# Performance work log

Measured on AMD Instinct MI355X. Metric: run time of the kernel, lower is better.

Reference implementation:

```python
import jax, jax.numpy as jnp
import numpy as np

B, D_IN, D_H = 4096, 1024, 1024


def setup_inputs() -> dict:
    key = jax.random.key(0)
    ks = jax.random.split(key, 11)
    s = 1.0 / np.sqrt(D_IN + D_H)  # torch Linear default init scale
    inp = {
        "x": jax.random.normal(ks[0], (B, D_IN), jnp.float32),
        "h": jax.random.normal(ks[1], (B, D_H), jnp.float32),
        "c": jax.random.normal(ks[2], (B, D_H), jnp.float32),
        "W_f": jax.random.uniform(ks[3], (D_IN + D_H, D_H), jnp.float32, -s, s),
        "b_f": jax.random.uniform(ks[4], (D_H,), jnp.float32, -s, s),
        "W_i": jax.random.uniform(ks[5], (D_IN + D_H, D_H), jnp.float32, -s, s),
        "b_i": jax.random.uniform(ks[6], (D_H,), jnp.float32, -s, s),
        "W_c": jax.random.uniform(ks[7], (D_IN + D_H, D_H), jnp.float32, -s, s),
        "b_c": jax.random.uniform(ks[8], (D_H,), jnp.float32, -s, s),
        "W_o": jax.random.uniform(ks[9], (D_IN + D_H, D_H), jnp.float32, -s, s),
        "b_o": jax.random.uniform(ks[10], (D_H,), jnp.float32, -s, s),
    }
    return inp


def reference(x, h, c, W_f, b_f, W_i, b_i, W_c, b_c, W_o, b_o):
    xh = jnp.concatenate([x, h], axis=1)  # [B, D_IN+D_H]
    # fuse four gate linears into one GEMM: [B, 2H] @ [2H, 4H]
    W = jnp.concatenate([W_f, W_i, W_c, W_o], axis=1)
    b = jnp.concatenate([b_f, b_i, b_c, b_o], axis=0)
    gates = xh @ W + b  # [B, 4H]
    f_g, i_g, c_g, o_g = jnp.split(gates, 4, axis=1)
    f = jax.nn.sigmoid(f_g)
    i = jax.nn.sigmoid(i_g)
    ct = jnp.tanh(c_g)
    ot = jax.nn.sigmoid(o_g)
    c_new = f * c + i * ct
    h_new = ot * jnp.tanh(c_new)
    return (h_new, (h_new, c_new))
```

## Files before the change

### kernel.cpp

```cpp
#include <hip/hip_runtime.h>
#include <hip/hip_bf16.h>
#include <cstdint>

typedef __bf16 bf16x8 __attribute__((ext_vector_type(8)));
typedef float f32x4 __attribute__((ext_vector_type(4)));

#define BROWS 4096
#define DH    1024
#define KDIM  2048
#define NT    32

__global__ __launch_bounds__(256) void k_prep(const float* __restrict__ x,
                                              const float* __restrict__ h,
                                              const float* __restrict__ Wf,
                                              const float* __restrict__ Wi,
                                              const float* __restrict__ Wc,
                                              const float* __restrict__ Wo,
                                              __hip_bfloat16* __restrict__ xh,
                                              __hip_bfloat16* __restrict__ wt) {
  __shared__ float t[64][65];
  const int tid = threadIdx.x;
  if (blockIdx.x < 4096) {
    int64_t idx = ((int64_t)blockIdx.x * 256 + tid) * 8;
    int row = (int)(idx >> 11);
    int col = (int)(idx & 2047);
    const float* src = (col < 1024) ? (x + (int64_t)row * 1024 + col)
                                    : (h + (int64_t)row * 1024 + (col - 1024));
    float4 v0 = reinterpret_cast<const float4*>(src)[0];
    float4 v1 = reinterpret_cast<const float4*>(src)[1];
    alignas(16) __hip_bfloat16 o8[8];
    o8[0] = __float2bfloat16(v0.x); o8[1] = __float2bfloat16(v0.y);
    o8[2] = __float2bfloat16(v0.z); o8[3] = __float2bfloat16(v0.w);
    o8[4] = __float2bfloat16(v1.x); o8[5] = __float2bfloat16(v1.y);
    o8[6] = __float2bfloat16(v1.z); o8[7] = __float2bfloat16(v1.w);
    *reinterpret_cast<int4*>(xh + idx) = *reinterpret_cast<const int4*>(o8);
  } else {
    const int b = blockIdx.x - 4096;
    const int g  = b & 3;
    const int jt = (b >> 2) & 15;
    const int kt = b >> 6;
    const float* W = (g == 0) ? Wf : (g == 1) ? Wi : (g == 2) ? Wc : Wo;
    const int j0 = jt << 6, k0 = kt << 6;
#pragma unroll
    for (int i = 0; i < 4; ++i) {
      int r = (tid >> 4) + (i << 4);
      int c = (tid & 15) << 2;
      float4 v = *reinterpret_cast<const float4*>(W + (int64_t)(k0 + r) * 1024 + j0 + c);
      t[r][c + 0] = v.x; t[r][c + 1] = v.y; t[r][c + 2] = v.z; t[r][c + 3] = v.w;
    }
    __syncthreads();
#pragma unroll
    for (int i = 0; i < 2; ++i) {
      int task = tid + (i << 8);
      int rr = task >> 3;
      int kc = (task & 7) << 3;
      int np = (((jt << 2) + (rr >> 4)) << 6) + (g << 4) + (rr & 15);
      alignas(16) __hip_bfloat16 o8[8];
#pragma unroll
      for (int e = 0; e < 8; ++e) o8[e] = __float2bfloat16(t[kc + e][rr]);
      *reinterpret_cast<int4*>(wt + (int64_t)np * KDIM + k0 + kc) =
          *reinterpret_cast<const int4*>(o8);
    }
  }
}

__device__ __forceinline__ float sig_(float v) {
  return __builtin_amdgcn_rcpf(1.0f + __expf(-v));
}
__device__ __forceinline__ float tanh_(float v) {
  return fmaf(2.0f, __builtin_amdgcn_rcpf(1.0f + __expf(-2.0f * v)), -1.0f);
}

#define GLD(PTR, LOFF)                                                           \
  __builtin_amdgcn_global_load_lds(                                              \
      (const __attribute__((address_space(1))) void*)(PTR),                      \
      (__attribute__((address_space(3))) void*)(lds + (LOFF) + wslot), 16, 0, 0)

#define STG2(LP, KH_, PA, PB)                                                    \
  do {                                                                           \
    GLD((PA), (LP) + (KH_) * 8192);                                              \
    GLD((PA) + 128 * KDIM, (LP) + (KH_) * 8192 + 4096);                          \
    GLD((PB), (LP) + 16384 + (KH_) * 8192);                                      \
    GLD((PB) + 128 * KDIM, (LP) + 16384 + (KH_) * 8192 + 4096);                  \
  } while (0)

#define LDSA(P, KH, MI)                                                          \
  (*reinterpret_cast<const bf16x8*>(lds + (P) * 32768 + (KH) * 8192 + abase + (MI) * 512))
#define LDSB(P, KH, NI)                                                          \
  (*reinterpret_cast<const bf16x8*>(lds + (P) * 32768 + (KH) * 8192 + bbase + (NI) * 512))

#define VM4 asm volatile("s_waitcnt vmcnt(4)" ::: "memory")

#define RD_AV(BANK, P_, KH_, H_)                                                 \
  _Pragma("unroll") for (int i = 0; i < 4; ++i) BANK[i] = LDSA(P_, KH_, (H_) * 4 + i)
#define RD_BV(P_, KH_)                                                           \
  _Pragma("unroll") for (int ni = 0; ni < 4; ++ni) bv[ni] = LDSB(P_, KH_, ni)

#define MM(BANK, MIH_)                                                           \
  do {                                                                           \
    __builtin_amdgcn_s_setprio(1);                                               \
    _Pragma("unroll") for (int i = 0; i < 4; ++i)                                \
      _Pragma("unroll") for (int ni = 0; ni < 4; ++ni)                           \
        acc[(MIH_) * 4 + i][ni] = __builtin_amdgcn_mfma_f32_16x16x32_bf16(       \
            BANK[i], bv[ni], acc[(MIH_) * 4 + i][ni], 0, 0, 0);                  \
    __builtin_amdgcn_s_setprio(0);                                               \
    __builtin_amdgcn_s_barrier();                                                \
  } while (0)

#define ADV do { a0 += 64; b0 += 64; } while (0)

__global__ __launch_bounds__(512, 2) void k_lstm_gemm(
    const __hip_bfloat16* __restrict__ xh, const __hip_bfloat16* __restrict__ wt,
    const float* __restrict__ cin,
    const float* __restrict__ bfp, const float* __restrict__ bip,
    const float* __restrict__ bcp, const float* __restrict__ bop,
    float* __restrict__ out) {
  __shared__ __hip_bfloat16 lds[65536];
  const int tid  = threadIdx.x;
  const int lane = tid & 63;
  const int wid  = tid >> 6;
  const int wm = wid >> 2, wn = wid & 3;
  const int wmb = wm << 7, wnb = wn << 6;

  const int bid  = blockIdx.x;
  const int flat = ((bid & 7) << 5) | (bid >> 3);
  const int m0 = (flat & 15) << 8;
  const int n0 = (flat >> 4) << 8;

  f32x4 acc[8][4] = {};

  const int wslot = wid << 9;
  const int cl = (((lane & 3) ^ ((lane >> 3) & 3)) << 3);
  const __hip_bfloat16* a0 = xh + (int64_t)(m0 + (tid >> 2)) * KDIM + cl;
  const __hip_bfloat16* b0 = wt + (int64_t)(n0 + (tid >> 2)) * KDIM + cl;

  const int frow = lane & 15;
  const int rx   = (((lane >> 4) ^ ((frow >> 1) & 3)) << 3);
  const int abase = ((wmb + frow) << 5) + rx;
  const int bbase = 16384 + ((wnb + frow) << 5) + rx;

  bf16x8 avA[4], avB[4], bv[4];

  STG2(0, 0, a0, b0);
  STG2(0, 1, a0 + 32, b0 + 32);
  ADV;
  VM4;
  __builtin_amdgcn_s_barrier();
  RD_AV(avA, 0, 0, 0);

  for (int t = 0; t < NT; t += 2) {
    {
      RD_BV(0, 0); RD_AV(avB, 0, 0, 1);
      STG2(32768, 0, a0, b0);
      VM4; MM(avA, 0);
      RD_AV(avA, 0, 1, 0);
      STG2(32768, 1, a0 + 32, b0 + 32);
      MM(avB, 1);
      RD_BV(0, 1); RD_AV(avB, 0, 1, 1);
      VM4; MM(avA, 0);
      RD_AV(avA, 1, 0, 0);
      MM(avB, 1);
    }
    if (t != 30) ADV;
    {
      RD_BV(1, 0); RD_AV(avB, 1, 0, 1);
      STG2(0, 0, a0, b0);
      VM4; MM(avA, 0);
      RD_AV(avA, 1, 1, 0);
      STG2(0, 1, a0 + 32, b0 + 32);
      MM(avB, 1);
      RD_BV(1, 1); RD_AV(avB, 1, 1, 1);
      VM4; MM(avA, 0);
      RD_AV(avA, 0, 0, 0);
      MM(avB, 1);
    }
    ADV;
  }

  const int j = (((n0 >> 6) + wn) << 4) + frow;
  const float vbf = bfp[j], vbi = bip[j], vbc = bcp[j], vbo = bop[j];
  const int q4 = (lane >> 4) << 2;
  float* outh1 = out;
  float* outh2 = out + (int64_t)BROWS * DH;
  float* outc  = out + (int64_t)2 * BROWS * DH;
#pragma unroll
  for (int mi = 0; mi < 8; ++mi) {
    const int mbase = m0 + wmb + (mi << 4) + q4;
#pragma unroll
    for (int r = 0; r < 4; ++r) {
      const int m = mbase + r;
      const int64_t idx = (int64_t)m * DH + j;
      float fg = sig_(acc[mi][0][r] + vbf);
      float ig = sig_(acc[mi][1][r] + vbi);
      float cg = tanh_(acc[mi][2][r] + vbc);
      float og = sig_(acc[mi][3][r] + vbo);
      float cn = fg * cin[idx] + ig * cg;
      float hn = og * tanh_(cn);
      outh1[idx] = hn;
      outh2[idx] = hn;
      outc[idx]  = cn;
    }
  }
}

extern "C" void kernel_launch(void* const* d_in, const int* in_sizes, int n_in,
                              void* d_out, int out_size, void* d_ws, size_t ws_size,
                              hipStream_t stream) {
  const float* x  = (const float*)d_in[0];
  const float* h  = (const float*)d_in[1];
  const float* c  = (const float*)d_in[2];
  const float* Wf = (const float*)d_in[3];
  const float* bf = (const float*)d_in[4];
  const float* Wi = (const float*)d_in[5];
  const float* bi = (const float*)d_in[6];
  const float* Wc = (const float*)d_in[7];
  const float* bc = (const float*)d_in[8];
  const float* Wo = (const float*)d_in[9];
  const float* bo = (const float*)d_in[10];
  float* out = (float*)d_out;

  __hip_bfloat16* xh = (__hip_bfloat16*)d_ws;
  __hip_bfloat16* wt = xh + (int64_t)BROWS * KDIM;

  hipLaunchKernelGGL(k_prep, dim3(6144), dim3(256), 0, stream,
                     x, h, Wf, Wi, Wc, Wo, xh, wt);
  hipLaunchKernelGGL(k_lstm_gemm, dim3(256), dim3(512), 0, stream,
                     xh, wt, c, bf, bi, bc, bo, out);
}
```

Before: 87.66 us.

## Switch LSTM GEMM to 32x32x16 MFMA with 4x2 wave tiling

Result: slower. 98.56 us (+12.4%).

```diff
diff --git a/kernel.cpp b/kernel.cpp
--- a/kernel.cpp
+++ b/kernel.cpp
@@ -3,7 +3,7 @@
 #include <cstdint>
 
 typedef __bf16 bf16x8 __attribute__((ext_vector_type(8)));
-typedef float f32x4 __attribute__((ext_vector_type(4)));
+typedef float f32x16 __attribute__((ext_vector_type(16)));
 
 #define BROWS 4096
 #define DH    1024
@@ -54,7 +54,7 @@
       int task = tid + (i << 8);
       int rr = task >> 3;
       int kc = (task & 7) << 3;
-      int np = (((jt << 2) + (rr >> 4)) << 6) + (g << 4) + (rr & 15);
+      int np = ((jt * 2 + (rr >> 5)) << 7) + (g << 5) + (rr & 31);
       alignas(16) __hip_bfloat16 o8[8];
 #pragma unroll
       for (int e = 0; e < 8; ++e) o8[e] = __float2bfloat16(t[kc + e][rr]);
@@ -84,25 +84,41 @@
     GLD((PB) + 128 * KDIM, (LP) + 16384 + (KH_) * 8192 + 4096);                  \
   } while (0)
 
-#define LDSA(P, KH, MI)                                                          \
-  (*reinterpret_cast<const bf16x8*>(lds + (P) * 32768 + (KH) * 8192 + abase + (MI) * 512))
-#define LDSB(P, KH, NI)                                                          \
-  (*reinterpret_cast<const bf16x8*>(lds + (P) * 32768 + (KH) * 8192 + bbase + (NI) * 512))
-
 #define VM4 asm volatile("s_waitcnt vmcnt(4)" ::: "memory")
-
-#define RD_AV(BANK, P_, KH_, H_)                                                 \
-  _Pragma("unroll") for (int i = 0; i < 4; ++i) BANK[i] = LDSA(P_, KH_, (H_) * 4 + i)
-#define RD_BV(P_, KH_)                                                           \
-  _Pragma("unroll") for (int ni = 0; ni < 4; ++ni) bv[ni] = LDSB(P_, KH_, ni)
-
-#define MM(BANK, MIH_)                                                           \
-  do {                                                                           \
+#define SB0 __builtin_amdgcn_sched_barrier(0)
+
+#define RD_AV(P, KH)                                                             \
+  do {                                                                           \
+    const __hip_bfloat16* _b = lds + (P) * 32768 + (KH) * 8192 + arow;           \
+    av[0] = *reinterpret_cast<const bf16x8*>(_b + c0);                           \
+    av[1] = *reinterpret_cast<const bf16x8*>(_b + c1);                           \
+    av[2] = *reinterpret_cast<const bf16x8*>(_b + 1024 + c0);                    \
+    av[3] = *reinterpret_cast<const bf16x8*>(_b + 1024 + c1);                    \
+  } while (0)
+
+#define RD_BV(P, KH, NH)                                                         \
+  do {                                                                           \
+    const __hip_bfloat16* _b = lds + (P) * 32768 + (KH) * 8192 + brow + (NH) * 2048; \
+    bv[0] = *reinterpret_cast<const bf16x8*>(_b + c0);                           \
+    bv[1] = *reinterpret_cast<const bf16x8*>(_b + c1);                           \
+    bv[2] = *reinterpret_cast<const bf16x8*>(_b + 1024 + c0);                    \
+    bv[3] = *reinterpret_cast<const bf16x8*>(_b + 1024 + c1);                    \
+  } while (0)
+
+#define MFMA32(A_, B_, C_) __builtin_amdgcn_mfma_f32_32x32x16_bf16(A_, B_, C_, 0, 0, 0)
+
+#define MM8(NH)                                                                  \
+  do {                                                                           \
+    __builtin_amdgcn_s_barrier();                                                \
     __builtin_amdgcn_s_setprio(1);                                               \
-    _Pragma("unroll") for (int i = 0; i < 4; ++i)                                \
-      _Pragma("unroll") for (int ni = 0; ni < 4; ++ni)                           \
-        acc[(MIH_) * 4 + i][ni] = __builtin_amdgcn_mfma_f32_16x16x32_bf16(       \
-            BANK[i], bv[ni], acc[(MIH_) * 4 + i][ni], 0, 0, 0);                  \
+    acc[0][2 * (NH)]     = MFMA32(av[0], bv[0], acc[0][2 * (NH)]);               \
+    acc[0][2 * (NH) + 1] = MFMA32(av[0], bv[2], acc[0][2 * (NH) + 1]);           \
+    acc[1][2 * (NH)]     = MFMA32(av[2], bv[0], acc[1][2 * (NH)]);               \
+    acc[1][2 * (NH) + 1] = MFMA32(av[2], bv[2], acc[1][2 * (NH) + 1]);           \
+    acc[0][2 * (NH)]     = MFMA32(av[1], bv[1], acc[0][2 * (NH)]);               \
+    acc[0][2 * (NH) + 1] = MFMA32(av[1], bv[3], acc[0][2 * (NH) + 1]);           \
+    acc[1][2 * (NH)]     = MFMA32(av[3], bv[1], acc[1][2 * (NH)]);               \
+    acc[1][2 * (NH) + 1] = MFMA32(av[3], bv[3], acc[1][2 * (NH) + 1]);           \
     __builtin_amdgcn_s_setprio(0);                                               \
     __builtin_amdgcn_s_barrier();                                                \
   } while (0)
@@ -119,81 +135,81 @@
   const int tid  = threadIdx.x;
   const int lane = tid & 63;
   const int wid  = tid >> 6;
-  const int wm = wid >> 2, wn = wid & 3;
-  const int wmb = wm << 7, wnb = wn << 6;
+  const int wm = wid >> 1, wn = wid & 1;
 
   const int bid  = blockIdx.x;
   const int flat = ((bid & 7) << 5) | (bid >> 3);
   const int m0 = (flat & 15) << 8;
   const int n0 = (flat >> 4) << 8;
 
-  f32x4 acc[8][4] = {};
+  f32x16 acc[2][4] = {};
 
   const int wslot = wid << 9;
   const int cl = (((lane & 3) ^ ((lane >> 3) & 3)) << 3);
   const __hip_bfloat16* a0 = xh + (int64_t)(m0 + (tid >> 2)) * KDIM + cl;
   const __hip_bfloat16* b0 = wt + (int64_t)(n0 + (tid >> 2)) * KDIM + cl;
 
-  const int frow = lane & 15;
-  const int rx   = (((lane >> 4) ^ ((frow >> 1) & 3)) << 3);
-  const int abase = ((wmb + frow) << 5) + rx;
-  const int bbase = 16384 + ((wnb + frow) << 5) + rx;
-
-  bf16x8 avA[4], avB[4], bv[4];
+  const int r5  = lane & 31;
+  const int hi  = lane >> 5;
+  const int lsw = (r5 >> 1) & 3;
+  const int c0  = (hi ^ lsw) << 3;
+  const int c1  = ((2 + hi) ^ lsw) << 3;
+  const int arow = (wm * 64 + r5) << 5;
+  const int brow = 16384 + ((wn * 128 + r5) << 5);
+
+  bf16x8 av[4], bv[4];
 
   STG2(0, 0, a0, b0);
   STG2(0, 1, a0 + 32, b0 + 32);
   ADV;
   VM4;
   __builtin_amdgcn_s_barrier();
-  RD_AV(avA, 0, 0, 0);
 
   for (int t = 0; t < NT; t += 2) {
     {
-      RD_BV(0, 0); RD_AV(avB, 0, 0, 1);
+      RD_AV(0, 0); RD_BV(0, 0, 0); SB0;
       STG2(32768, 0, a0, b0);
-      VM4; MM(avA, 0);
-      RD_AV(avA, 0, 1, 0);
+      VM4; MM8(0);
+      RD_BV(0, 0, 1); SB0;
       STG2(32768, 1, a0 + 32, b0 + 32);
-      MM(avB, 1);
-      RD_BV(0, 1); RD_AV(avB, 0, 1, 1);
-      VM4; MM(avA, 0);
-      RD_AV(avA, 1, 0, 0);
-      MM(avB, 1);
+      MM8(1);
+      RD_AV(0, 1); RD_BV(0, 1, 0); SB0;
+      VM4; MM8(0);
+      RD_BV(0, 1, 1); SB0;
+      MM8(1);
     }
     if (t != 30) ADV;
     {
-      RD_BV(1, 0); RD_AV(avB, 1, 0, 1);
+      RD_AV(1, 0); RD_BV(1, 0, 0); SB0;
       STG2(0, 0, a0, b0);
-      VM4; MM(avA, 0);
-      RD_AV(avA, 1, 1, 0);
+      VM4; MM8(0);
+      RD_BV(1, 0, 1); SB0;
       STG2(0, 1, a0 + 32, b0 + 32);
-      MM(avB, 1);
-      RD_BV(1, 1); RD_AV(avB, 1, 1, 1);
-      VM4; MM(avA, 0);
-      RD_AV(avA, 0, 0, 0);
-      MM(avB, 1);
+      MM8(1);
+      RD_AV(1, 1); RD_BV(1, 1, 0); SB0;
+      VM4; MM8(0);
+      RD_BV(1, 1, 1); SB0;
+      MM8(1);
     }
     ADV;
   }
 
-  const int j = (((n0 >> 6) + wn) << 4) + frow;
+  const int j = (((n0 >> 7) + wn) << 5) + r5;
   const float vbf = bfp[j], vbi = bip[j], vbc = bcp[j], vbo = bop[j];
-  const int q4 = (lane >> 4) << 2;
+  const int mb0 = m0 + wm * 64 + (hi << 2);
   float* outh1 = out;
   float* outh2 = out + (int64_t)BROWS * DH;
   float* outc  = out + (int64_t)2 * BROWS * DH;
 #pragma unroll
-  for (int mi = 0; mi < 8; ++mi) {
-    const int mbase = m0 + wmb + (mi << 4) + q4;
-#pragma unroll
-    for (int r = 0; r < 4; ++r) {
-      const int m = mbase + r;
+  for (int mt = 0; mt < 2; ++mt) {
+#pragma unroll
+    for (int reg = 0; reg < 16; ++reg) {
+      const int m = mb0 + mt * 32 + (reg & 3) + ((reg >> 2) << 3);
       const int64_t idx = (int64_t)m * DH + j;
-      float fg = sig_(acc[mi][0][r] + vbf);
-      float ig = sig_(acc[mi][1][r] + vbi);
-      float cg = tanh_(acc[mi][2][r] + vbc);
-      float og = sig_(acc[mi][3][r] + vbo);
+      float fg = sig_(acc[mt][0][reg] + vbf);
+      float ig = sig_(acc[mt][1][reg] + vbi);
+      float cg = tanh_(acc[mt][2][reg] + vbc);
+      float og = sig_(acc[mt][3][reg] + vbo);
       float cn = fg * cin[idx] + ig * cg;
       float hn = og * tanh_(cn);
       outh1[idx] = hn;
```
